# Optimization experiments

Hardware: AMD Instinct MI355X
Metric: run time of the kernel (lower is better)

## Reference

```python
import jax, jax.numpy as jnp
import numpy as np

B, L, D, K = 32, 128, 400, 40
RTOL, ATOL = 1e-4, 1e-6


def setup_inputs() -> dict:
    key = jax.random.key(0)
    ks = jax.random.split(key, 9)
    s = 0.3                      # input scale keeps exp(energy) in fp32 range
    u = 1.0 / np.sqrt(D)         # param scale
    input_h = jax.random.normal(ks[0], (B, L, D), jnp.float32) * s
    input_c = jax.random.normal(ks[1], (B, L, D), jnp.float32) * s
    W_d = jax.random.normal(ks[2], (K, D), jnp.float32) * u
    W_e = jax.random.normal(ks[3], (K, D), jnp.float32) * u
    U = jax.random.normal(ks[4], (K, D, D), jnp.float32) * u
    b = jax.random.normal(ks[5], (K,), jnp.float32) * 0.1
    heads = jax.random.randint(ks[6], (B, L), 0, L)
    pos = jnp.arange(L)[None, :]
    heads = jnp.where(heads == pos, (heads + 1) % L, heads)  # no self-loops (diag is -inf)
    arc_tags = jax.random.randint(ks[7], (B, L), 0, K)
    lengths = jax.random.randint(ks[8], (B,), L // 2, L + 1)
    mask = (jnp.arange(L)[None, :] < lengths[:, None]).astype(jnp.float32)
    return {"input_h": input_h, "input_c": input_c, "W_d": W_d, "W_e": W_e,
            "U": U, "b": b, "mask": mask, "heads": heads,
            "arc_tags": arc_tags, "lengths": lengths}


def reference(input_h, input_c, W_d, W_e, U, b, mask, heads, arc_tags, lengths):
    Bsz, Ln, _ = input_h.shape
    # --- BiAAttention: energy[b,k,head,child] ---
    bil = jnp.einsum('bhd,kde,bce->bkhc', input_h, U, input_c)
    sd = jnp.einsum('kd,bhd->bkh', W_d, input_h)[:, :, :, None]   # head bias
    se = jnp.einsum('kd,bcd->bkc', W_e, input_c)[:, :, None, :]   # child bias
    energy = bil + sd + se + b[None, :, None, None]
    energy = energy * mask[:, None, :, None] * mask[:, None, None, :]
    eye = jnp.eye(Ln, dtype=energy.dtype)
    energy = energy + jnp.where(eye > 0, -jnp.inf, 0.0)           # no self-arcs
    # --- Matrix-Tree partition function ---
    A = jnp.exp(energy) * mask[:, None, :, None] * mask[:, None, None, :]
    A = A.sum(axis=1)                                             # [B,L,L] over labels
    Dg = A.sum(axis=1) * (1.0 + RTOL) + ATOL                      # column (in-degree) sums
    Lap = eye * Dg[:, None, :] - A                                # Laplacian
    Sub = Lap[:, 1:, 1:]                                          # drop root row/col
    valid = jnp.arange(Ln - 1)[None, :] < (lengths - 1)[:, None]
    vm = valid[:, :, None] & valid[:, None, :]
    Sub = jnp.where(vm, Sub, jnp.eye(Ln - 1, dtype=Sub.dtype))    # identity-pad = logdet of [1:len,1:len]
    z = jnp.linalg.slogdet(Sub)[1]                                # [B]
    # --- gold-tree energy ---
    bi = jnp.arange(Bsz)[:, None]
    pos = jnp.arange(Ln)[None, :]
    te = energy[bi, arc_tags, heads, pos]                         # [B,L]
    tgt = te[:, 1:].sum(axis=1)
    return z - tgt
```

## Files before the change

kernel.cpp:

```cpp
#include <hip/hip_runtime.h>
#include <hip/hip_bf16.h>

#define BB 32
#define LL 128
#define DD 400
#define KK 40
#define EE 416
#define SDN 50
#define SEN 52

typedef __attribute__((ext_vector_type(8)))  short  bfrag;
typedef __attribute__((ext_vector_type(16))) float  ffrag;

static __device__ __forceinline__ short f2bf(float f) {
    union { float f; unsigned u; } v; v.f = f;
    unsigned r = (v.u + 0x7FFF + ((v.u >> 16) & 1)) >> 16;
    return (short)r;
}

__global__ __launch_bounds__(256) void p_hc(
    const float* __restrict__ H, const float* __restrict__ C,
    short* __restrict__ Hs, short* __restrict__ Cs)
{
    int id = blockIdx.x * 256 + threadIdx.x;
    if (id < BB*SDN*LL) {
        int b = id / (SDN*LL); int r = id % (SDN*LL);
        int sd = r / LL; int h = r % LL;
        const float* src = H + ((size_t)(b*LL + h))*DD + sd*8;
        bfrag v;
#pragma unroll
        for (int j = 0; j < 8; ++j) v[j] = f2bf(src[j]);
        *(bfrag*)(Hs + (size_t)id*8) = v;
    } else {
        id -= BB*SDN*LL;
        int b = id / (SEN*LL); int r = id % (SEN*LL);
        int se = r / LL; int c = r % LL;
        bfrag v;
#pragma unroll
        for (int j = 0; j < 8; ++j) {
            int e = se*8 + j;
            v[j] = (e < DD) ? f2bf(C[((size_t)(b*LL + c))*DD + e]) : (short)0;
        }
        *(bfrag*)(Cs + (size_t)id*8) = v;
    }
}

__global__ __launch_bounds__(256) void p_u(
    const float* __restrict__ U, short* __restrict__ Us)
{
    int id = blockIdx.x * 256 + threadIdx.x;
    int k = id / (SDN*EE); int r = id % (SDN*EE);
    int sd = r / EE; int e = r % EE;
    bfrag v;
#pragma unroll
    for (int j = 0; j < 8; ++j)
        v[j] = (e < DD) ? f2bf(U[((size_t)k*DD + sd*8 + j)*DD + e]) : (short)0;
    *(bfrag*)(Us + (size_t)id*8) = v;
}

__global__ __launch_bounds__(256) void k_sdse(
    const float* __restrict__ H, const float* __restrict__ C,
    const float* __restrict__ Wd, const float* __restrict__ We,
    float* __restrict__ SD, float* __restrict__ SE)
{
    const int k = blockIdx.x % KK;
    const int b = blockIdx.x / KK;
    const int t = threadIdx.x;
    __shared__ float wd[DD], we[DD];
    for (int f = t; f < DD; f += 256) { wd[f] = Wd[k*DD + f]; we[f] = We[k*DD + f]; }
    __syncthreads();
    const int row = t & 127;
    const float* src = (t < 128) ? (H + (size_t)(b*LL + row)*DD)
                                 : (C + (size_t)(b*LL + row)*DD);
    const float* w = (t < 128) ? wd : we;
    float s = 0.f;
    for (int d = 0; d < DD; d += 4) {
        float4 v = *(const float4*)(src + d);
        s = fmaf(v.x, w[d+0], s); s = fmaf(v.y, w[d+1], s);
        s = fmaf(v.z, w[d+2], s); s = fmaf(v.w, w[d+3], s);
    }
    if (t < 128) SD[(b*KK + k)*LL + row] = s;
    else         SE[(b*KK + k)*LL + row] = s;
}

__global__ __launch_bounds__(256, 2) void k_mfma(
    const short* __restrict__ Hs, const short* __restrict__ Cs,
    const short* __restrict__ Us,
    const float* __restrict__ SD, const float* __restrict__ SE,
    const float* __restrict__ bvec, const float* __restrict__ mask,
    const int* __restrict__ heads, const int* __restrict__ tags,
    float* __restrict__ A8, float* __restrict__ tgt)
{
    const int k = blockIdx.x;
    const int b = blockIdx.y;
    const int t = threadIdx.x;
    const int w  = t >> 6;
    const int l  = t & 63;
    const int l31 = l & 31;
    const int kh  = l >> 5;
    const int wm  = w >> 1;
    const int wn  = w & 1;

    __shared__ short Tbuf[16*LL*8];

    ffrag Sacc[2][2];
#pragma unroll
    for (int a = 0; a < 2; ++a)
#pragma unroll
        for (int c2 = 0; c2 < 2; ++c2)
#pragma unroll
            for (int r = 0; r < 16; ++r) Sacc[a][c2][r] = 0.f;

    const size_t usK = (size_t)k * SDN * EE;
    const size_t hsB = (size_t)b * SDN * LL;
    const size_t csB = (size_t)b * SEN * LL;

    for (int chunk = 0; chunk < 4; ++chunk) {
        const int e0  = chunk * 128;
        const int NEc = (chunk < 3) ? 128 : 32;
        const int nmt = (NEc == 128) ? 2 : ((wm == 0) ? 1 : 0);

        ffrag Tacc[2][2];
#pragma unroll
        for (int a = 0; a < 2; ++a)
#pragma unroll
            for (int c2 = 0; c2 < 2; ++c2)
#pragma unroll
                for (int r = 0; r < 16; ++r) Tacc[a][c2][r] = 0.f;

        if (nmt > 0) {
            for (int ds = 0; ds < 25; ++ds) {
                const int sdl = 2*ds + kh;
                bfrag afr[2], bfr[2];
#pragma unroll
                for (int mt = 0; mt < 2; ++mt) {
                    if (mt < nmt) {
                        int eg = e0 + 64*wm + 32*mt + l31;
                        afr[mt] = *(const bfrag*)(Us + (usK + (size_t)sdl*EE + eg)*8);
                    }
                }
#pragma unroll
                for (int nt = 0; nt < 2; ++nt) {
                    int h = 64*wn + 32*nt + l31;
                    bfr[nt] = *(const bfrag*)(Hs + (hsB + (size_t)sdl*LL + h)*8);
                }
#pragma unroll
                for (int mt = 0; mt < 2; ++mt) {
                    if (mt < nmt) {
#pragma unroll
                        for (int nt = 0; nt < 2; ++nt)
                            Tacc[mt][nt] = __builtin_amdgcn_mfma_f32_32x32x16_bf16(
                                afr[mt], bfr[nt], Tacc[mt][nt], 0, 0, 0);
                    }
                }
            }
#pragma unroll
            for (int mt = 0; mt < 2; ++mt) {
                if (mt < nmt) {
#pragma unroll
                    for (int nt = 0; nt < 2; ++nt) {
                        int h = 64*wn + 32*nt + l31;
#pragma unroll
                        for (int r = 0; r < 16; r += 2) {
                            int e_loc = 64*wm + 32*mt + (r&3) + 8*(r>>2) + 4*kh;
                            int s_e = e_loc >> 3, e7 = e_loc & 7;
                            unsigned lo = (unsigned short)f2bf(Tacc[mt][nt][r]);
                            unsigned hi = (unsigned short)f2bf(Tacc[mt][nt][r+1]);
                            *(unsigned*)(&Tbuf[((size_t)s_e*LL + h)*8 + e7]) =
                                lo | (hi << 16);
                        }
                    }
                }
            }
        }
        __syncthreads();

        const int esteps = NEc >> 4;
        for (int es = 0; es < esteps; ++es) {
            const int sel = 2*es + kh;
            bfrag afr[2], bfr[2];
#pragma unroll
            for (int at = 0; at < 2; ++at) {
                int h = 64*wm + 32*at + l31;
                afr[at] = *(const bfrag*)(&Tbuf[((size_t)sel*LL + h)*8]);
            }
#pragma unroll
            for (int bt = 0; bt < 2; ++bt) {
                int c = 64*wn + 32*bt + l31;
                int seg = (e0 >> 3) + sel;
                bfr[bt] = *(const bfrag*)(Cs + (csB + (size_t)seg*LL + c)*8);
            }
#pragma unroll
            for (int at = 0; at < 2; ++at)
#pragma unroll
                for (int bt = 0; bt < 2; ++bt)
                    Sacc[at][bt] = __builtin_amdgcn_mfma_f32_32x32x16_bf16(
                        afr[at], bfr[bt], Sacc[at][bt], 0, 0, 0);
        }
        __syncthreads();
    }

    const float bk = bvec[k];
    const float* SDb = SD + ((size_t)b*KK + k)*LL;
    const float* SEb = SE + ((size_t)b*KK + k)*LL;
    float* Ab = A8 + ((size_t)((k & 7)*BB + b))*LL*LL;

#pragma unroll
    for (int at = 0; at < 2; ++at) {
#pragma unroll
        for (int bt = 0; bt < 2; ++bt) {
            const int c = 64*wn + 32*bt + l31;
            const float mc = mask[b*LL + c];
            const float sev = SEb[c];
            const int headc = heads[b*LL + c];
            const int tagc  = tags[b*LL + c];
#pragma unroll
            for (int r = 0; r < 16; ++r) {
                int h = 64*wm + 32*at + (r&3) + 8*(r>>2) + 4*kh;
                if (h == c) continue;
                float mh = mask[b*LL + h];
                if (mh == 0.f || mc == 0.f) continue;
                float eng = Sacc[at][bt][r] + SDb[h] + sev + bk;
                atomicAdd(&Ab[h*LL + c], __expf(eng));
                if (c >= 1 && tagc == k && headc == h) atomicAdd(&tgt[b], eng);
            }
        }
    }
}

__global__ __launch_bounds__(256) void k_logdet(
    const float* __restrict__ A8, const int* __restrict__ lengths,
    const float* __restrict__ tgt, float* __restrict__ out)
{
    const int b = blockIdx.x;
    const int t = threadIdx.x;
    const int rg = t >> 4;
    const int cg = t & 15;

    __shared__ float As[LL*LL];
    __shared__ float Dg[128];
    __shared__ float Lbuf[128];
    __shared__ float Ubuf[128];
    __shared__ float red[256];

    const float4* A4 = (const float4*)A8;
    for (int f4 = t; f4 < 4096; f4 += 256) {
        float4 s = make_float4(0.f, 0.f, 0.f, 0.f);
#pragma unroll
        for (int g = 0; g < 8; ++g) {
            float4 v = A4[((size_t)(g*BB + b))*4096 + f4];
            s.x += v.x; s.y += v.y; s.z += v.z; s.w += v.w;
        }
        ((float4*)As)[f4] = s;
    }
    __syncthreads();

    if (t < 128) {
        float s = 0.f;
        for (int hr = 0; hr < LL; ++hr) s += As[hr*LL + t];
        Dg[t] = s * (1.0f + 1e-4f) + 1e-6f;
    }
    __syncthreads();

    const int n1 = lengths[b] - 1;
    float m[8][8];
#pragma unroll
    for (int r = 0; r < 8; ++r) {
        const int i = 8*rg + r;
#pragma unroll
        for (int c = 0; c < 8; ++c) {
            const int j = 8*cg + c;
            float v;
            if (i < n1 && j < n1)
                v = ((i == j) ? Dg[i+1] : 0.f) - As[(i+1)*LL + (j+1)];
            else
                v = (i == j) ? 1.f : 0.f;
            m[r][c] = v;
        }
    }
    __syncthreads();

    for (int j = 0; j < 127; ++j) {
        const int jg = j >> 3, jl = j & 7;
        if (cg == jg) {
#pragma unroll
            for (int c = 0; c < 8; ++c) {
                if (c == jl) {
#pragma unroll
                    for (int r = 0; r < 8; ++r) Lbuf[8*rg + r] = m[r][c];
                }
            }
        }
        if (rg == jg) {
#pragma unroll
            for (int r = 0; r < 8; ++r) {
                if (r == jl) {
#pragma unroll
                    for (int c = 0; c < 8; ++c) Ubuf[8*cg + c] = m[r][c];
                }
            }
        }
        __syncthreads();

        const float piv = Lbuf[j];
        if (t == j) Dg[j] = piv;
        const float rp = 1.0f / piv;
        float lr[8], ur[8];
#pragma unroll
        for (int r = 0; r < 8; ++r) lr[r] = Lbuf[8*rg + r] * rp;
#pragma unroll
        for (int c = 0; c < 8; ++c) ur[c] = Ubuf[8*cg + c];
#pragma unroll
        for (int r = 0; r < 8; ++r)
#pragma unroll
            for (int c = 0; c < 8; ++c)
                m[r][c] = fmaf(-lr[r], ur[c], m[r][c]);
        __syncthreads();
    }

    float lsum = 0.f;
    if (t < 127) lsum = logf(Dg[t]);
    red[t] = lsum;
    __syncthreads();
    for (int off = 128; off >= 1; off >>= 1) {
        if (t < off) red[t] += red[t + off];
        __syncthreads();
    }
    if (t == 0) out[b] = red[0] - tgt[b];
}

extern "C" void kernel_launch(void* const* d_in, const int* in_sizes, int n_in,
                              void* d_out, int out_size, void* d_ws, size_t ws_size,
                              hipStream_t stream) {
    const float* H    = (const float*)d_in[0];
    const float* C    = (const float*)d_in[1];
    const float* Wd   = (const float*)d_in[2];
    const float* We   = (const float*)d_in[3];
    const float* U    = (const float*)d_in[4];
    const float* bv   = (const float*)d_in[5];
    const float* mask = (const float*)d_in[6];
    const int* heads  = (const int*)d_in[7];
    const int* tags   = (const int*)d_in[8];
    const int* lens   = (const int*)d_in[9];
    float* out = (float*)d_out;

    char* p = (char*)d_ws;
    float* A8  = (float*)p;                 p += (size_t)8*BB*LL*LL*4;
    float* tgt = (float*)p;                 p += 32*4;
    float* SDp = (float*)p;                 p += (size_t)BB*KK*LL*4;
    float* SEp = (float*)p;                 p += (size_t)BB*KK*LL*4;
    short* Hsp = (short*)p;                 p += (size_t)BB*SDN*LL*8*2;
    short* Csp = (short*)p;                 p += (size_t)BB*SEN*LL*8*2;
    short* Usp = (short*)p;                 p += (size_t)KK*SDN*EE*8*2;

    hipMemsetAsync(d_ws, 0, ((size_t)8*BB*LL*LL + 32)*4, stream);

    p_hc  <<<dim3(1632), 256, 0, stream>>>(H, C, Hsp, Csp);
    p_u   <<<dim3(3250), 256, 0, stream>>>(U, Usp);
    k_sdse<<<dim3(BB*KK), 256, 0, stream>>>(H, C, Wd, We, SDp, SEp);
    k_mfma<<<dim3(KK, BB), 256, 0, stream>>>(Hsp, Csp, Usp, SDp, SEp, bv, mask,
                                             heads, tags, A8, tgt);
    k_logdet<<<dim3(BB), 256, 0, stream>>>(A8, lens, tgt, out);
}
```

Before: 413.9 us.

## Accumulate label groups in registers, drop atomics and memset, restructure sdse

The bilinear MFMA kernel now handles five labels per block (grid 8xB, 512 threads). It sums exp(energy) in registers and writes the A8 slices with plain stores, so the per-element atomicAdds and the large workspace memset go away. The inner MFMA loops are software-pipelined with explicit fragment prefetching, and validity masks are precomputed as bitmasks. The SD/SE bias kernel is reorganised so each thread computes all 40 labels for a quarter of one row, using shuffle reduction. The trade-off is fewer blocks (256) with more serial work per block, which may lower occupancy and parallelism.

```diff
diff --git a/kernel.cpp b/kernel.cpp
--- a/kernel.cpp
+++ b/kernel.cpp
@@ -18,6 +18,8 @@
     return (short)r;
 }
 
+#define MFMA32(a, b, c) __builtin_amdgcn_mfma_f32_32x32x16_bf16((a), (b), (c), 0, 0, 0)
+
 __global__ __launch_bounds__(256) void p_hc(
     const float* __restrict__ H, const float* __restrict__ C,
     short* __restrict__ Hs, short* __restrict__ Cs)
@@ -63,27 +65,41 @@
     const float* __restrict__ Wd, const float* __restrict__ We,
     float* __restrict__ SD, float* __restrict__ SE)
 {
-    const int k = blockIdx.x % KK;
-    const int b = blockIdx.x / KK;
+    const int b   = blockIdx.x;
+    const int src = blockIdx.y;
+    const int rg  = blockIdx.z;
     const int t = threadIdx.x;
-    __shared__ float wd[DD], we[DD];
-    for (int f = t; f < DD; f += 256) { wd[f] = Wd[k*DD + f]; we[f] = We[k*DD + f]; }
-    __syncthreads();
-    const int row = t & 127;
-    const float* src = (t < 128) ? (H + (size_t)(b*LL + row)*DD)
-                                 : (C + (size_t)(b*LL + row)*DD);
-    const float* w = (t < 128) ? wd : we;
-    float s = 0.f;
-    for (int d = 0; d < DD; d += 4) {
-        float4 v = *(const float4*)(src + d);
-        s = fmaf(v.x, w[d+0], s); s = fmaf(v.y, w[d+1], s);
-        s = fmaf(v.z, w[d+2], s); s = fmaf(v.w, w[d+3], s);
-    }
-    if (t < 128) SD[(b*KK + k)*LL + row] = s;
-    else         SE[(b*KK + k)*LL + row] = s;
-}
-
-__global__ __launch_bounds__(256, 2) void k_mfma(
+    const int row = rg*64 + (t >> 2);
+    const int q = t & 3;
+    const float* __restrict__ X = (src == 0 ? H : C) + ((size_t)(b*LL + row))*DD + q*100;
+    const float* __restrict__ W = (src == 0 ? Wd : We) + q*100;
+    float acc[KK];
+#pragma unroll
+    for (int k = 0; k < KK; ++k) acc[k] = 0.f;
+    for (int dc = 0; dc < 25; ++dc) {
+        float4 v = *(const float4*)(X + 4*dc);
+#pragma unroll
+        for (int k = 0; k < KK; ++k) {
+            float4 wv = *(const float4*)(W + (size_t)k*DD + 4*dc);
+            acc[k] = fmaf(v.x, wv.x, acc[k]);
+            acc[k] = fmaf(v.y, wv.y, acc[k]);
+            acc[k] = fmaf(v.z, wv.z, acc[k]);
+            acc[k] = fmaf(v.w, wv.w, acc[k]);
+        }
+    }
+#pragma unroll
+    for (int k = 0; k < KK; ++k) {
+        acc[k] += __shfl_xor(acc[k], 1);
+        acc[k] += __shfl_xor(acc[k], 2);
+    }
+    if (q == 0) {
+        float* out = (src == 0 ? SD : SE) + ((size_t)b*KK)*LL + row;
+#pragma unroll
+        for (int k = 0; k < KK; ++k) out[k*LL] = acc[k];
+    }
+}
+
+__global__ __launch_bounds__(512, 2) void k_mfma(
     const short* __restrict__ Hs, const short* __restrict__ Cs,
     const short* __restrict__ Us,
     const float* __restrict__ SD, const float* __restrict__ SE,
@@ -91,140 +107,153 @@
     const int* __restrict__ heads, const int* __restrict__ tags,
     float* __restrict__ A8, float* __restrict__ tgt)
 {
-    const int k = blockIdx.x;
+    const int g = blockIdx.x;
     const int b = blockIdx.y;
     const int t = threadIdx.x;
     const int w  = t >> 6;
     const int l  = t & 63;
     const int l31 = l & 31;
     const int kh  = l >> 5;
-    const int wm  = w >> 1;
-    const int wn  = w & 1;
+    const int et = w >> 1;
+    const int hh = w & 1;
+    const int ht = w >> 1;
+    const int ch = w & 1;
 
     __shared__ short Tbuf[16*LL*8];
 
-    ffrag Sacc[2][2];
-#pragma unroll
-    for (int a = 0; a < 2; ++a)
-#pragma unroll
-        for (int c2 = 0; c2 < 2; ++c2)
-#pragma unroll
-            for (int r = 0; r < 16; ++r) Sacc[a][c2][r] = 0.f;
-
-    const size_t usK = (size_t)k * SDN * EE;
     const size_t hsB = (size_t)b * SDN * LL;
     const size_t csB = (size_t)b * SEN * LL;
 
-    for (int chunk = 0; chunk < 4; ++chunk) {
-        const int e0  = chunk * 128;
-        const int NEc = (chunk < 3) ? 128 : 32;
-        const int nmt = (NEc == 128) ? 2 : ((wm == 0) ? 1 : 0);
-
-        ffrag Tacc[2][2];
-#pragma unroll
-        for (int a = 0; a < 2; ++a)
-#pragma unroll
-            for (int c2 = 0; c2 < 2; ++c2)
-#pragma unroll
-                for (int r = 0; r < 16; ++r) Tacc[a][c2][r] = 0.f;
-
-        if (nmt > 0) {
-            for (int ds = 0; ds < 25; ++ds) {
-                const int sdl = 2*ds + kh;
-                bfrag afr[2], bfr[2];
-#pragma unroll
-                for (int mt = 0; mt < 2; ++mt) {
-                    if (mt < nmt) {
-                        int eg = e0 + 64*wm + 32*mt + l31;
-                        afr[mt] = *(const bfrag*)(Us + (usK + (size_t)sdl*EE + eg)*8);
-                    }
-                }
-#pragma unroll
-                for (int nt = 0; nt < 2; ++nt) {
-                    int h = 64*wn + 32*nt + l31;
-                    bfr[nt] = *(const bfrag*)(Hs + (hsB + (size_t)sdl*LL + h)*8);
-                }
-#pragma unroll
-                for (int mt = 0; mt < 2; ++mt) {
-                    if (mt < nmt) {
-#pragma unroll
-                        for (int nt = 0; nt < 2; ++nt)
-                            Tacc[mt][nt] = __builtin_amdgcn_mfma_f32_32x32x16_bf16(
-                                afr[mt], bfr[nt], Tacc[mt][nt], 0, 0, 0);
-                    }
+    const int hbase = 32*ht + 4*kh;
+    const int c0 = 64*ch + l31;
+    const int c1 = c0 + 32;
+    const float mc0 = mask[b*LL + c0], mc1 = mask[b*LL + c1];
+    const int head0 = heads[b*LL + c0], head1 = heads[b*LL + c1];
+    const int tag0  = tags[b*LL + c0],  tag1  = tags[b*LL + c1];
+    unsigned vb0 = 0, vb1 = 0;
+#pragma unroll
+    for (int r = 0; r < 16; ++r) {
+        const int hr = hbase + (r&3) + 8*(r>>2);
+        const float mh = mask[b*LL + hr];
+        if (mh != 0.f && mc0 != 0.f && hr != c0) vb0 |= 1u << r;
+        if (mh != 0.f && mc1 != 0.f && hr != c1) vb1 |= 1u << r;
+    }
+
+    ffrag E0, E1, S0, S1;
+#pragma unroll
+    for (int r = 0; r < 16; ++r) { E0[r] = 0.f; E1[r] = 0.f; }
+
+    for (int kk = 0; kk < 5; ++kk) {
+        const int k = g + 8*kk;
+        const size_t usK = (size_t)k * SDN * EE;
+#pragma unroll
+        for (int r = 0; r < 16; ++r) { S0[r] = 0.f; S1[r] = 0.f; }
+
+        for (int chunk = 0; chunk < 4; ++chunk) {
+            const int e0 = chunk << 7;
+            const bool tail = (chunk == 3);
+
+            if (!tail || et == 0) {
+                ffrag T0, T1;
+#pragma unroll
+                for (int r = 0; r < 16; ++r) { T0[r] = 0.f; T1[r] = 0.f; }
+                const short* up  = Us + (usK + (size_t)(e0 + 32*et + l31) + (size_t)kh*EE)*8;
+                const short* hp0 = Hs + (hsB + (size_t)(64*hh + l31) + (size_t)kh*LL)*8;
+                const short* hp1 = hp0 + 32*8;
+#define UF(i) (*(const bfrag*)(up  + (size_t)(i)*(2*EE*8)))
+#define XF(i) (*(const bfrag*)(hp0 + (size_t)(i)*(2*LL*8)))
+#define YF(i) (*(const bfrag*)(hp1 + (size_t)(i)*(2*LL*8)))
+                bfrag a0=UF(0), x0=XF(0), y0=YF(0);
+                bfrag a1=UF(1), x1=XF(1), y1=YF(1);
+                bfrag a2=UF(2), x2=XF(2), y2=YF(2);
+#pragma unroll 1
+                for (int j = 0; j < 8; ++j) {
+                    const int i0 = (3*j+3 < 25) ? 3*j+3 : 24;
+                    const int i1 = (3*j+4 < 25) ? 3*j+4 : 24;
+                    const int i2 = (3*j+5 < 25) ? 3*j+5 : 24;
+                    bfrag a3=UF(i0), x3=XF(i0), y3=YF(i0);
+                    bfrag a4=UF(i1), x4=XF(i1), y4=YF(i1);
+                    bfrag a5=UF(i2), x5=XF(i2), y5=YF(i2);
+                    T0 = MFMA32(a0, x0, T0); T1 = MFMA32(a0, y0, T1);
+                    T0 = MFMA32(a1, x1, T0); T1 = MFMA32(a1, y1, T1);
+                    T0 = MFMA32(a2, x2, T0); T1 = MFMA32(a2, y2, T1);
+                    a0=a3; x0=x3; y0=y3; a1=a4; x1=x4; y1=y4; a2=a5; x2=x5; y2=y5;
+                }
+                T0 = MFMA32(a0, x0, T0); T1 = MFMA32(a0, y0, T1);
+#undef UF
+#undef XF
+#undef YF
+                const int hA = 64*hh + l31;
+#pragma unroll
+                for (int r = 0; r < 16; r += 2) {
+                    const int e_loc = 32*et + (r&3) + 8*(r>>2) + 4*kh;
+                    const int s_e = e_loc >> 3, e7 = e_loc & 7;
+                    unsigned lo0 = (unsigned short)f2bf(T0[r]);
+                    unsigned hi0 = (unsigned short)f2bf(T0[r+1]);
+                    *(unsigned*)(&Tbuf[((size_t)s_e*LL + hA)*8 + e7]) = lo0 | (hi0 << 16);
+                    unsigned lo1 = (unsigned short)f2bf(T1[r]);
+                    unsigned hi1 = (unsigned short)f2bf(T1[r+1]);
+                    *(unsigned*)(&Tbuf[((size_t)s_e*LL + hA + 32)*8 + e7]) = lo1 | (hi1 << 16);
                 }
             }
-#pragma unroll
-            for (int mt = 0; mt < 2; ++mt) {
-                if (mt < nmt) {
-#pragma unroll
-                    for (int nt = 0; nt < 2; ++nt) {
-                        int h = 64*wn + 32*nt + l31;
-#pragma unroll
-                        for (int r = 0; r < 16; r += 2) {
-                            int e_loc = 64*wm + 32*mt + (r&3) + 8*(r>>2) + 4*kh;
-                            int s_e = e_loc >> 3, e7 = e_loc & 7;
-                            unsigned lo = (unsigned short)f2bf(Tacc[mt][nt][r]);
-                            unsigned hi = (unsigned short)f2bf(Tacc[mt][nt][r+1]);
-                            *(unsigned*)(&Tbuf[((size_t)s_e*LL + h)*8 + e7]) =
-                                lo | (hi << 16);
-                        }
-                    }
-                }
+            __syncthreads();
+
+            const short* tb  = Tbuf + ((size_t)(kh*LL) + 32*ht + l31)*8;
+            const short* cp0 = Cs + (csB + (size_t)((chunk*16 + kh)*LL) + 64*ch + l31)*8;
+            const short* cp1 = cp0 + 32*8;
+#define TF(es) (*(const bfrag*)(tb  + (size_t)(es)*(2*LL*8)))
+#define PF(es) (*(const bfrag*)(cp0 + (size_t)(es)*(2*LL*8)))
+#define QF(es) (*(const bfrag*)(cp1 + (size_t)(es)*(2*LL*8)))
+            if (!tail) {
+                bfrag t0=TF(0), u0=PF(0), v0=QF(0);
+                bfrag t1=TF(1), u1=PF(1), v1=QF(1);
+#pragma unroll 1
+                for (int it = 0; it < 3; ++it) {
+                    bfrag t2=TF(2*it+2), u2=PF(2*it+2), v2=QF(2*it+2);
+                    bfrag t3=TF(2*it+3), u3=PF(2*it+3), v3=QF(2*it+3);
+                    S0 = MFMA32(t0, u0, S0); S1 = MFMA32(t0, v0, S1);
+                    S0 = MFMA32(t1, u1, S0); S1 = MFMA32(t1, v1, S1);
+                    t0=t2; u0=u2; v0=v2; t1=t3; u1=u3; v1=v3;
+                }
+                S0 = MFMA32(t0, u0, S0); S1 = MFMA32(t0, v0, S1);
+                S0 = MFMA32(t1, u1, S0); S1 = MFMA32(t1, v1, S1);
+            } else {
+                bfrag t0=TF(0), u0=PF(0), v0=QF(0);
+                bfrag t1=TF(1), u1=PF(1), v1=QF(1);
+                S0 = MFMA32(t0, u0, S0); S1 = MFMA32(t0, v0, S1);
+                S0 = MFMA32(t1, u1, S0); S1 = MFMA32(t1, v1, S1);
             }
-        }
-        __syncthreads();
-
-        const int esteps = NEc >> 4;
-        for (int es = 0; es < esteps; ++es) {
-            const int sel = 2*es + kh;
-            bfrag afr[2], bfr[2];
-#pragma unroll
-            for (int at = 0; at < 2; ++at) {
-                int h = 64*wm + 32*at + l31;
-                afr[at] = *(const bfrag*)(&Tbuf[((size_t)sel*LL + h)*8]);
-            }
-#pragma unroll
-            for (int bt = 0; bt < 2; ++bt) {
-                int c = 64*wn + 32*bt + l31;
-                int seg = (e0 >> 3) + sel;
-                bfr[bt] = *(const bfrag*)(Cs + (csB + (size_t)seg*LL + c)*8);
-            }
-#pragma unroll
-            for (int at = 0; at < 2; ++at)
-#pragma unroll
-                for (int bt = 0; bt < 2; ++bt)
-                    Sacc[at][bt] = __builtin_amdgcn_mfma_f32_32x32x16_bf16(
-                        afr[at], bfr[bt], Sacc[at][bt], 0, 0, 0);
-        }
-        __syncthreads();
-    }
-
-    const float bk = bvec[k];
-    const float* SDb = SD + ((size_t)b*KK + k)*LL;
-    const float* SEb = SE + ((size_t)b*KK + k)*LL;
-    float* Ab = A8 + ((size_t)((k & 7)*BB + b))*LL*LL;
-
-#pragma unroll
-    for (int at = 0; at < 2; ++at) {
-#pragma unroll
-        for (int bt = 0; bt < 2; ++bt) {
-            const int c = 64*wn + 32*bt + l31;
-            const float mc = mask[b*LL + c];
-            const float sev = SEb[c];
-            const int headc = heads[b*LL + c];
-            const int tagc  = tags[b*LL + c];
-#pragma unroll
-            for (int r = 0; r < 16; ++r) {
-                int h = 64*wm + 32*at + (r&3) + 8*(r>>2) + 4*kh;
-                if (h == c) continue;
-                float mh = mask[b*LL + h];
-                if (mh == 0.f || mc == 0.f) continue;
-                float eng = Sacc[at][bt][r] + SDb[h] + sev + bk;
-                atomicAdd(&Ab[h*LL + c], __expf(eng));
-                if (c >= 1 && tagc == k && headc == h) atomicAdd(&tgt[b], eng);
-            }
-        }
+#undef TF
+#undef PF
+#undef QF
+            __syncthreads();
+        }
+
+        const float bk = bvec[k];
+        const float* SDb = SD + ((size_t)b*KK + k)*LL;
+        const float* SEb = SE + ((size_t)b*KK + k)*LL;
+        const float se0 = SEb[c0], se1 = SEb[c1];
+#pragma unroll
+        for (int r = 0; r < 16; ++r) {
+            const int hr = hbase + (r&3) + 8*(r>>2);
+            const float sdv = SDb[hr];
+            const float e0v = S0[r] + sdv + se0 + bk;
+            const float e1v = S1[r] + sdv + se1 + bk;
+            if ((vb0 >> r) & 1) E0[r] += __expf(e0v);
+            if ((vb1 >> r) & 1) E1[r] += __expf(e1v);
+            if (((vb0 >> r) & 1) && c0 >= 1 && tag0 == k && head0 == hr)
+                atomicAdd(&tgt[b], e0v);
+            if (((vb1 >> r) & 1) && c1 >= 1 && tag1 == k && head1 == hr)
+                atomicAdd(&tgt[b], e1v);
+        }
+    }
+
+    float* Ab = A8 + ((size_t)(g*BB + b))*LL*LL;
+#pragma unroll
+    for (int r = 0; r < 16; ++r) {
+        const int hr = hbase + (r&3) + 8*(r>>2);
+        Ab[hr*LL + c0] = E0[r];
+        Ab[hr*LL + c1] = E1[r];
     }
 }
 
@@ -353,12 +382,12 @@
     short* Csp = (short*)p;                 p += (size_t)BB*SEN*LL*8*2;
     short* Usp = (short*)p;                 p += (size_t)KK*SDN*EE*8*2;
 
-    hipMemsetAsync(d_ws, 0, ((size_t)8*BB*LL*LL + 32)*4, stream);
+    hipMemsetAsync(tgt, 0, 32*4, stream);
 
     p_hc  <<<dim3(1632), 256, 0, stream>>>(H, C, Hsp, Csp);
     p_u   <<<dim3(3250), 256, 0, stream>>>(U, Usp);
-    k_sdse<<<dim3(BB*KK), 256, 0, stream>>>(H, C, Wd, We, SDp, SEp);
-    k_mfma<<<dim3(KK, BB), 256, 0, stream>>>(Hsp, Csp, Usp, SDp, SEp, bv, mask,
-                                             heads, tags, A8, tgt);
+    k_sdse<<<dim3(BB, 2, 2), 256, 0, stream>>>(H, C, Wd, We, SDp, SEp);
+    k_mfma<<<dim3(8, BB), 512, 0, stream>>>(Hsp, Csp, Usp, SDp, SEp, bv, mask,
+                                            heads, tags, A8, tgt);
     k_logdet<<<dim3(BB), 256, 0, stream>>>(A8, lens, tgt, out);
 }
```

After: 448.2 us. 8.3% more time.
